# Optimization experiments

Measured on AMD Instinct MI355X. Metric: run time of the kernel, lower is better.

The kernel has to match this reference:

```python
import jax, jax.numpy as jnp
import numpy as np

N_NEWS = 200000
N_COMPANIES = 10000
N_EDGES = 640000
HIDDEN = 256


def setup_inputs() -> dict:
    key = jax.random.key(0)
    ks = jax.random.split(key, 7)
    scale = 1.0 / np.sqrt(HIDDEN)  # keep tanh out of full saturation
    news_x = jax.random.normal(ks[0], (N_NEWS, HIDDEN), dtype=jnp.float32)
    company_x = jax.random.normal(ks[1], (N_COMPANIES, HIDDEN), dtype=jnp.float32)
    W_news = jax.random.normal(ks[2], (HIDDEN, HIDDEN), dtype=jnp.float32) * scale
    W_company = jax.random.normal(ks[3], (HIDDEN, HIDDEN), dtype=jnp.float32) * scale
    v = jax.random.normal(ks[4], (HIDDEN,), dtype=jnp.float32) * scale
    src = jax.random.randint(ks[5], (N_EDGES,), 0, N_NEWS, dtype=jnp.int64)
    dst = jax.random.randint(ks[6], (N_EDGES,), 0, N_COMPANIES, dtype=jnp.int64)
    return {
        "news_x": news_x,
        "company_x": company_x,
        "W_news": W_news,
        "W_company": W_company,
        "v": v,
        "src": src,
        "dst": dst,
        "num_companies": N_COMPANIES,
    }


def reference(news_x, company_x, W_news, W_company, v, src, dst, num_companies):
    # Gather per-edge endpoint features, project (nn.Linear applies x @ W.T).
    news_part = news_x[src] @ W_news.T          # [E, H]
    company_part = company_x[dst] @ W_company.T  # [E, H]
    scores = jnp.tanh(news_part + company_part) @ v  # [E]

    # Segment-wise (per-company) numerically stable softmax over incoming edges.
    smax = jax.ops.segment_max(scores, dst, num_segments=num_companies)  # [C]
    scores_exp = jnp.exp(scores - smax[dst])                             # [E]
    denom = jax.ops.segment_sum(scores_exp, dst, num_segments=num_companies)[dst]
    weights = scores_exp / jnp.clip(denom, 1e-9)                         # [E]

    # Weighted scatter-add of raw news features into company slots.
    out = jax.ops.segment_sum(news_x[src] * weights[:, None], dst,
                              num_segments=num_companies)               # [C, H]
    return out
```

## Files before the change

### kernel.cpp

```cpp
#include <hip/hip_runtime.h>
#include <hip/hip_bf16.h>
#include <cmath>
#include <cstdint>


#define H 256

typedef __attribute__((ext_vector_type(8))) short bfrag;
typedef __attribute__((ext_vector_type(4))) float ffrag;

__device__ __forceinline__ ushort f2bf(float f) {
  uint u = __float_as_uint(f);
  uint r = u + 0x7FFFu + ((u >> 16) & 1u);
  return (ushort)(r >> 16);
}
__device__ __forceinline__ float bf2f(ushort h) {
  return __uint_as_float((uint)h << 16);
}

__global__ void prep_kernel(const float* __restrict__ Wn, const float* __restrict__ Wc,
                            ushort* __restrict__ WnHi, ushort* __restrict__ WnLo,
                            ushort* __restrict__ WcHi, ushort* __restrict__ WcLo,
                            const int* __restrict__ dst, int* __restrict__ counts, int E) {
  const int b = blockIdx.x, tid = threadIdx.x;
  if (b < 256) {
    int i = b * 256 + tid;
    float w = Wn[i];
    ushort h = f2bf(w);
    WnHi[i] = h;
    WnLo[i] = f2bf(w - bf2f(h));
  } else if (b < 512) {
    int i = (b - 256) * 256 + tid;
    float w = Wc[i];
    ushort h = f2bf(w);
    WcHi[i] = h;
    WcLo[i] = f2bf(w - bf2f(h));
  } else {
    int e = (b - 512) * 256 + tid;
    if (e < E) atomicAdd(&counts[dst[e]], 1);
  }
}

__global__ void scan_kernel(const int* __restrict__ counts, int* __restrict__ offsets,
                            int* __restrict__ cursor, int C) {
  __shared__ int wsum[16];
  int tid = threadIdx.x;
  int lane = tid & 63, wid = tid >> 6;
  int base = 0;
  for (int start = 0; start < C; start += 1024) {
    int idx = start + tid;
    int val = (idx < C) ? counts[idx] : 0;
    int x = val;
#pragma unroll
    for (int off = 1; off < 64; off <<= 1) {
      int y = __shfl_up(x, off);
      if (lane >= off) x += y;
    }
    if (lane == 63) wsum[wid] = x;
    __syncthreads();
    int add = base;
    for (int w = 0; w < wid; ++w) add += wsum[w];
    if (idx < C) {
      int excl = add + x - val;
      offsets[idx] = excl;
      cursor[idx]  = excl;
    }
    int tot = 0;
#pragma unroll
    for (int w = 0; w < 16; ++w) tot += wsum[w];
    __syncthreads();
    base += tot;
  }
  if (tid == 0) offsets[C] = base;
}

__global__ void fill_kernel(const int* __restrict__ src, const int* __restrict__ dst,
                            int* __restrict__ cursor, int* __restrict__ srcs_sorted, int E) {
  int e = blockIdx.x * blockDim.x + threadIdx.x;
  if (e < E) {
    int d = dst[e];
    int pos = atomicAdd(&cursor[d], 1);
    srcs_sorted[pos] = src[e];
  }
}

__global__ __launch_bounds__(256, 4) void gemm_fused(
    const float* __restrict__ Xc, const ushort* __restrict__ WcHi,
    const ushort* __restrict__ WcLo, ushort* __restrict__ cproj, int MC, int nbC,
    const float* __restrict__ Xn, const ushort* __restrict__ WnHi,
    const ushort* __restrict__ WnLo, ushort* __restrict__ nproj,
    ushort* __restrict__ nxbf, int MN) {
  constexpr int PITCH = 264;
  __shared__ ushort Xs[64 * PITCH];
  const int tid = threadIdx.x;
  const int wave = tid >> 6, lane = tid & 63;
  const int q = lane >> 4, nidx = lane & 15;

  const float* X; const ushort *Whi, *Wlo; ushort *proj, *xb; int M, row0;
  if ((int)blockIdx.x < nbC) {
    X = Xc; Whi = WcHi; Wlo = WcLo; proj = cproj; xb = nullptr;
    M = MC; row0 = blockIdx.x * 64;
  } else {
    X = Xn; Whi = WnHi; Wlo = WnLo; proj = nproj; xb = nxbf;
    M = MN; row0 = (blockIdx.x - nbC) * 64;
  }

#pragma unroll
  for (int it = 0; it < 8; ++it) {
    const int flat = it * 2048 + tid * 8;
    const int r = flat >> 8, k = flat & 255;
    int gr = row0 + r;
    if (gr >= M) gr = M - 1;
    const float4 x0 = *(const float4*)(X + (size_t)gr * H + k);
    const float4 x1 = *(const float4*)(X + (size_t)gr * H + k + 4);
    bfrag xc;
    xc[0] = (short)f2bf(x0.x); xc[1] = (short)f2bf(x0.y);
    xc[2] = (short)f2bf(x0.z); xc[3] = (short)f2bf(x0.w);
    xc[4] = (short)f2bf(x1.x); xc[5] = (short)f2bf(x1.y);
    xc[6] = (short)f2bf(x1.z); xc[7] = (short)f2bf(x1.w);
    *(bfrag*)&Xs[r * PITCH + k] = xc;
    if (xb) *(bfrag*)(xb + (size_t)gr * H + k) = xc;
  }
  __syncthreads();

  ffrag acc[4][4];
#pragma unroll
  for (int i = 0; i < 4; ++i)
#pragma unroll
    for (int t = 0; t < 4; ++t) acc[i][t] = (ffrag)(0.f);

#pragma unroll
  for (int ks = 0; ks < 8; ++ks) {
    const int k0 = ks * 32;
    bfrag a[4];
#pragma unroll
    for (int i = 0; i < 4; ++i)
      a[i] = *(const bfrag*)&Xs[(16 * i + nidx) * PITCH + k0 + q * 8];
    bfrag bhi[4], blo[4];
#pragma unroll
    for (int t = 0; t < 4; ++t) {
      const size_t off = (size_t)(wave * 64 + t * 16 + nidx) * H + k0 + q * 8;
      bhi[t] = *(const bfrag*)(Whi + off);
      blo[t] = *(const bfrag*)(Wlo + off);
    }
#pragma unroll
    for (int i = 0; i < 4; ++i)
#pragma unroll
      for (int t = 0; t < 4; ++t) {
        acc[i][t] = __builtin_amdgcn_mfma_f32_16x16x32_bf16(a[i], bhi[t], acc[i][t], 0, 0, 0);
        acc[i][t] = __builtin_amdgcn_mfma_f32_16x16x32_bf16(a[i], blo[t], acc[i][t], 0, 0, 0);
      }
  }

#pragma unroll
  for (int i = 0; i < 4; ++i)
#pragma unroll
    for (int r = 0; r < 4; ++r) {
      const int grow = row0 + 16 * i + q * 4 + r;
      if (grow < M) {
#pragma unroll
        for (int t = 0; t < 4; ++t)
          proj[(size_t)grow * H + wave * 64 + t * 16 + nidx] = f2bf(acc[i][t][r]);
      }
    }
}

__device__ __forceinline__ float fast_tanh(float x) {
  float e = __expf(2.f * x);
  return 1.f - 2.f / (e + 1.f);
}

__device__ __forceinline__ float score_dot(ushort4 p, float4 cq, float4 vv) {
  float r = fast_tanh(bf2f(p.x) + cq.x) * vv.x + fast_tanh(bf2f(p.y) + cq.y) * vv.y +
            fast_tanh(bf2f(p.z) + cq.z) * vv.z + fast_tanh(bf2f(p.w) + cq.w) * vv.w;
#pragma unroll
  for (int off = 32; off > 0; off >>= 1) r += __shfl_xor(r, off);
  return r;
}

__global__ __launch_bounds__(256) void edge_flash_kernel(
    const ushort* __restrict__ news_projbf, const ushort* __restrict__ company_projbf,
    const float* __restrict__ v, const int* __restrict__ offsets,
    const int* __restrict__ srcs, const ushort* __restrict__ news_xbf,
    float* __restrict__ out) {
  const int c = blockIdx.x;
  const int tid = threadIdx.x, lane = tid & 63, wid = tid >> 6;
  __shared__ float cp[H];
  __shared__ float mW[4], lW[4];
  __shared__ float OW[4][H];
  cp[tid] = bf2f(company_projbf[(size_t)c * H + tid]);
  __syncthreads();
  const float4 vv = *(const float4*)(v + lane * 4);
  const float4 cq = *(const float4*)&cp[lane * 4];
  const int beg = offsets[c], end = offsets[c + 1];

  float m = -INFINITY, l = 0.f;
  float4 O = make_float4(0.f, 0.f, 0.f, 0.f);

  int i = beg + wid * 2;
  if (i + 1 < end) {
    int s0 = srcs[i], s1 = srcs[i + 1];
    ushort4 p0 = *(const ushort4*)(news_projbf + (size_t)s0 * H + lane * 4);
    ushort4 p1 = *(const ushort4*)(news_projbf + (size_t)s1 * H + lane * 4);
    ushort4 x0 = *(const ushort4*)(news_xbf + (size_t)s0 * H + lane * 4);
    ushort4 x1 = *(const ushort4*)(news_xbf + (size_t)s1 * H + lane * 4);
    for (;;) {
      const int inext = i + 8;
      const bool more = (inext + 1 < end);
      ushort4 np0, np1, nx0, nx1;
      if (more) {
        int t0 = srcs[inext], t1 = srcs[inext + 1];
        np0 = *(const ushort4*)(news_projbf + (size_t)t0 * H + lane * 4);
        np1 = *(const ushort4*)(news_projbf + (size_t)t1 * H + lane * 4);
        nx0 = *(const ushort4*)(news_xbf + (size_t)t0 * H + lane * 4);
        nx1 = *(const ushort4*)(news_xbf + (size_t)t1 * H + lane * 4);
      }
      const float sa = score_dot(p0, cq, vv);
      const float sb = score_dot(p1, cq, vv);
      const float mnew = fmaxf(m, fmaxf(sa, sb));
      const float alpha = __expf(m - mnew);
      const float pa = __expf(sa - mnew);
      const float pb = __expf(sb - mnew);
      l = l * alpha + pa + pb;
      O.x = O.x * alpha + pa * bf2f(x0.x) + pb * bf2f(x1.x);
      O.y = O.y * alpha + pa * bf2f(x0.y) + pb * bf2f(x1.y);
      O.z = O.z * alpha + pa * bf2f(x0.z) + pb * bf2f(x1.z);
      O.w = O.w * alpha + pa * bf2f(x0.w) + pb * bf2f(x1.w);
      m = mnew;
      i = inext;
      if (!more) break;
      p0 = np0; p1 = np1; x0 = nx0; x1 = nx1;
    }
  }
  if (i < end) {
    const int s0 = srcs[i];
    const ushort4 p0 = *(const ushort4*)(news_projbf + (size_t)s0 * H + lane * 4);
    const ushort4 x0 = *(const ushort4*)(news_xbf + (size_t)s0 * H + lane * 4);
    const float sa = score_dot(p0, cq, vv);
    const float mnew = fmaxf(m, sa);
    const float alpha = __expf(m - mnew);
    const float pa = __expf(sa - mnew);
    l = l * alpha + pa;
    O.x = O.x * alpha + pa * bf2f(x0.x);
    O.y = O.y * alpha + pa * bf2f(x0.y);
    O.z = O.z * alpha + pa * bf2f(x0.z);
    O.w = O.w * alpha + pa * bf2f(x0.w);
    m = mnew;
  }

  if (lane == 0) { mW[wid] = m; lW[wid] = l; }
  *(float4*)&OW[wid][lane * 4] = O;
  __syncthreads();
  const float mstar = fmaxf(fmaxf(mW[0], mW[1]), fmaxf(mW[2], mW[3]));
  float denom = 0.f, val = 0.f;
#pragma unroll
  for (int w = 0; w < 4; ++w) {
    const float sc = (lW[w] > 0.f) ? __expf(mW[w] - mstar) : 0.f;
    denom += lW[w] * sc;
    val += OW[w][tid] * sc;
  }
  out[(size_t)c * H + tid] = val / fmaxf(denom, 1e-9f);
}

extern "C" void kernel_launch(void* const* d_in, const int* in_sizes, int n_in,
                              void* d_out, int out_size, void* d_ws, size_t ws_size,
                              hipStream_t stream) {
  const float* news_x    = (const float*)d_in[0];
  const float* company_x = (const float*)d_in[1];
  const float* W_news    = (const float*)d_in[2];
  const float* W_company = (const float*)d_in[3];
  const float* v         = (const float*)d_in[4];
  const int*   src       = (const int*)d_in[5];
  const int*   dst       = (const int*)d_in[6];
  const int N = in_sizes[0] / H;
  const int C = in_sizes[1] / H;
  const int E = in_sizes[5];
  float* out = (float*)d_out;

  char* p = (char*)d_ws;
  ushort* news_projbf    = (ushort*)p; p += (size_t)N * H * sizeof(ushort);
  ushort* news_xbf       = (ushort*)p; p += (size_t)N * H * sizeof(ushort);
  ushort* company_projbf = (ushort*)p; p += (size_t)C * H * sizeof(ushort);
  int*    srcs_sorted    = (int*)p;    p += (size_t)E * sizeof(int);
  ushort* Wn_hi          = (ushort*)p; p += (size_t)H * H * sizeof(ushort);
  ushort* Wn_lo          = (ushort*)p; p += (size_t)H * H * sizeof(ushort);
  ushort* Wc_hi          = (ushort*)p; p += (size_t)H * H * sizeof(ushort);
  ushort* Wc_lo          = (ushort*)p; p += (size_t)H * H * sizeof(ushort);
  int*    counts         = (int*)p;    p += (size_t)C * sizeof(int);
  int*    offsets        = (int*)p;    p += (size_t)(C + 1) * sizeof(int);
  int*    cursor         = (int*)p;    p += (size_t)C * sizeof(int);

  hipMemsetAsync(counts, 0, (size_t)C * sizeof(int), stream);
  prep_kernel<<<512 + (E + 255) / 256, 256, 0, stream>>>(
      W_news, W_company, Wn_hi, Wn_lo, Wc_hi, Wc_lo, dst, counts, E);
  scan_kernel<<<1, 1024, 0, stream>>>(counts, offsets, cursor, C);
  fill_kernel<<<(E + 255) / 256, 256, 0, stream>>>(src, dst, cursor, srcs_sorted, E);

  const int nbC = (C + 63) / 64, nbN = (N + 63) / 64;
  gemm_fused<<<nbC + nbN, 256, 0, stream>>>(
      company_x, Wc_hi, Wc_lo, company_projbf, C, nbC,
      news_x, Wn_hi, Wn_lo, news_projbf, news_xbf, N);

  edge_flash_kernel<<<C, 256, 0, stream>>>(news_projbf, company_projbf, v, offsets,
                                           srcs_sorted, news_xbf, out);
}
```

Baseline: 629.9 us.

## Make projection GEMM persistent with register-resident weights and double-buffered tiles

```diff
diff --git a/kernel.cpp b/kernel.cpp
--- a/kernel.cpp
+++ b/kernel.cpp
@@ -84,85 +84,112 @@
   }
 }
 
-__global__ __launch_bounds__(256, 4) void gemm_fused(
+__global__ __launch_bounds__(512, 2) void gemm_persist(
     const float* __restrict__ Xc, const ushort* __restrict__ WcHi,
-    const ushort* __restrict__ WcLo, ushort* __restrict__ cproj, int MC, int nbC,
+    const ushort* __restrict__ WcLo, ushort* __restrict__ cproj, int MC, int GC,
     const float* __restrict__ Xn, const ushort* __restrict__ WnHi,
     const ushort* __restrict__ WnLo, ushort* __restrict__ nproj,
     ushort* __restrict__ nxbf, int MN) {
   constexpr int PITCH = 264;
-  __shared__ ushort Xs[64 * PITCH];
+  __shared__ ushort Xs[2][64 * PITCH];
   const int tid = threadIdx.x;
-  const int wave = tid >> 6, lane = tid & 63;
+  const int wv = tid >> 6, lane = tid & 63;
   const int q = lane >> 4, nidx = lane & 15;
-
-  const float* X; const ushort *Whi, *Wlo; ushort *proj, *xb; int M, row0;
-  if ((int)blockIdx.x < nbC) {
-    X = Xc; Whi = WcHi; Wlo = WcLo; proj = cproj; xb = nullptr;
-    M = MC; row0 = blockIdx.x * 64;
+  const int GN = gridDim.x - GC;
+
+  const float* X; const ushort *Whi, *Wlo; ushort *proj, *xb; int M, nb, lb;
+  if ((int)blockIdx.x < GC) {
+    X = Xc; Whi = WcHi; Wlo = WcLo; proj = cproj; xb = nullptr; M = MC;
+    nb = GC; lb = blockIdx.x;
   } else {
-    X = Xn; Whi = WnHi; Wlo = WnLo; proj = nproj; xb = nxbf;
-    M = MN; row0 = (blockIdx.x - nbC) * 64;
-  }
-
-#pragma unroll
-  for (int it = 0; it < 8; ++it) {
-    const int flat = it * 2048 + tid * 8;
-    const int r = flat >> 8, k = flat & 255;
-    int gr = row0 + r;
-    if (gr >= M) gr = M - 1;
-    const float4 x0 = *(const float4*)(X + (size_t)gr * H + k);
-    const float4 x1 = *(const float4*)(X + (size_t)gr * H + k + 4);
-    bfrag xc;
-    xc[0] = (short)f2bf(x0.x); xc[1] = (short)f2bf(x0.y);
-    xc[2] = (short)f2bf(x0.z); xc[3] = (short)f2bf(x0.w);
-    xc[4] = (short)f2bf(x1.x); xc[5] = (short)f2bf(x1.y);
-    xc[6] = (short)f2bf(x1.z); xc[7] = (short)f2bf(x1.w);
-    *(bfrag*)&Xs[r * PITCH + k] = xc;
-    if (xb) *(bfrag*)(xb + (size_t)gr * H + k) = xc;
-  }
-  __syncthreads();
-
-  ffrag acc[4][4];
-#pragma unroll
-  for (int i = 0; i < 4; ++i)
-#pragma unroll
-    for (int t = 0; t < 4; ++t) acc[i][t] = (ffrag)(0.f);
-
-#pragma unroll
-  for (int ks = 0; ks < 8; ++ks) {
-    const int k0 = ks * 32;
-    bfrag a[4];
+    X = Xn; Whi = WnHi; Wlo = WnLo; proj = nproj; xb = nxbf; M = MN;
+    nb = GN; lb = blockIdx.x - GC;
+  }
+  const int nt = (M + 63) >> 6;
+  const int qt = nt / nb, rt = nt % nb;
+  const int first = lb * qt + (lb < rt ? lb : rt);
+  const int cnt = qt + (lb < rt ? 1 : 0);
+  if (cnt <= 0) return;
+
+  bfrag bhi[8][2], blo[8][2];
+#pragma unroll
+  for (int ks = 0; ks < 8; ++ks)
+#pragma unroll
+    for (int tt = 0; tt < 2; ++tt) {
+      const size_t off = (size_t)(wv * 32 + tt * 16 + nidx) * H + ks * 32 + q * 8;
+      bhi[ks][tt] = *(const bfrag*)(Whi + off);
+      blo[ks][tt] = *(const bfrag*)(Wlo + off);
+    }
+
+  float4 xr[8];
+  auto load8 = [&](int tile) {
+#pragma unroll
+    for (int j = 0; j < 8; ++j) {
+      const int flat = j * 2048 + tid * 4;
+      int gr = tile * 64 + (flat >> 8);
+      if (gr >= M) gr = M - 1;
+      xr[j] = *(const float4*)(X + (size_t)gr * H + (flat & 255));
+    }
+  };
+  auto writebuf = [&](int p, int tile) {
+#pragma unroll
+    for (int j = 0; j < 8; ++j) {
+      const int flat = j * 2048 + tid * 4;
+      const int r = flat >> 8, k = flat & 255;
+      ushort4 b4;
+      b4.x = f2bf(xr[j].x); b4.y = f2bf(xr[j].y);
+      b4.z = f2bf(xr[j].z); b4.w = f2bf(xr[j].w);
+      *(ushort4*)&Xs[p][r * PITCH + k] = b4;
+      if (xb) {
+        const int gr = tile * 64 + r;
+        *(ushort4*)(xb + (size_t)gr * H + k) = b4;
+      }
+    }
+  };
+
+  load8(first);
+  writebuf(0, first);
+  int p = 0;
+  for (int t = 0; t < cnt; ++t) {
+    __syncthreads();
+    const int tile = first + t;
+    const bool more = (t + 1 < cnt);
+    if (more) load8(tile + 1);
+
+    ffrag acc[4][2];
+#pragma unroll
+    for (int i = 0; i < 4; ++i) { acc[i][0] = (ffrag)(0.f); acc[i][1] = (ffrag)(0.f); }
+#pragma unroll
+    for (int ks = 0; ks < 8; ++ks) {
+      bfrag a[4];
+#pragma unroll
+      for (int i = 0; i < 4; ++i)
+        a[i] = *(const bfrag*)&Xs[p][(16 * i + nidx) * PITCH + ks * 32 + q * 8];
+#pragma unroll
+      for (int i = 0; i < 4; ++i)
+#pragma unroll
+        for (int tt = 0; tt < 2; ++tt) {
+          acc[i][tt] = __builtin_amdgcn_mfma_f32_16x16x32_bf16(a[i], bhi[ks][tt], acc[i][tt], 0, 0, 0);
+          acc[i][tt] = __builtin_amdgcn_mfma_f32_16x16x32_bf16(a[i], blo[ks][tt], acc[i][tt], 0, 0, 0);
+        }
+    }
+
+    const int row0 = tile * 64;
 #pragma unroll
     for (int i = 0; i < 4; ++i)
-      a[i] = *(const bfrag*)&Xs[(16 * i + nidx) * PITCH + k0 + q * 8];
-    bfrag bhi[4], blo[4];
-#pragma unroll
-    for (int t = 0; t < 4; ++t) {
-      const size_t off = (size_t)(wave * 64 + t * 16 + nidx) * H + k0 + q * 8;
-      bhi[t] = *(const bfrag*)(Whi + off);
-      blo[t] = *(const bfrag*)(Wlo + off);
-    }
-#pragma unroll
-    for (int i = 0; i < 4; ++i)
-#pragma unroll
-      for (int t = 0; t < 4; ++t) {
-        acc[i][t] = __builtin_amdgcn_mfma_f32_16x16x32_bf16(a[i], bhi[t], acc[i][t], 0, 0, 0);
-        acc[i][t] = __builtin_amdgcn_mfma_f32_16x16x32_bf16(a[i], blo[t], acc[i][t], 0, 0, 0);
+#pragma unroll
+      for (int r = 0; r < 4; ++r) {
+        const int grow = row0 + 16 * i + q * 4 + r;
+        if (grow < M) {
+#pragma unroll
+          for (int tt = 0; tt < 2; ++tt)
+            proj[(size_t)grow * H + wv * 32 + tt * 16 + nidx] = f2bf(acc[i][tt][r]);
+        }
       }
-  }
-
-#pragma unroll
-  for (int i = 0; i < 4; ++i)
-#pragma unroll
-    for (int r = 0; r < 4; ++r) {
-      const int grow = row0 + 16 * i + q * 4 + r;
-      if (grow < M) {
-#pragma unroll
-        for (int t = 0; t < 4; ++t)
-          proj[(size_t)grow * H + wave * 64 + t * 16 + nidx] = f2bf(acc[i][t][r]);
-      }
-    }
+
+    if (more) writebuf(p ^ 1, tile + 1);
+    p ^= 1;
+  }
 }
 
 __device__ __forceinline__ float fast_tanh(float x) {
@@ -296,9 +323,9 @@
   scan_kernel<<<1, 1024, 0, stream>>>(counts, offsets, cursor, C);
   fill_kernel<<<(E + 255) / 256, 256, 0, stream>>>(src, dst, cursor, srcs_sorted, E);
 
-  const int nbC = (C + 63) / 64, nbN = (N + 63) / 64;
-  gemm_fused<<<nbC + nbN, 256, 0, stream>>>(
-      company_x, Wc_hi, Wc_lo, company_projbf, C, nbC,
+  const int GC = 24, GN = 488;
+  gemm_persist<<<GC + GN, 512, 0, stream>>>(
+      company_x, Wc_hi, Wc_lo, company_projbf, C, GC,
       news_x, Wn_hi, Wn_lo, news_projbf, news_xbf, N);
 
   edge_flash_kernel<<<C, 256, 0, stream>>>(news_projbf, company_projbf, v, offsets,
```

Measured after the change: 556.1 us. 1.13x faster.
